# Optimization experiments

Measured on AMD Instinct MI355X. Metric: run time of the kernel, lower is better.

The kernel has to match this reference:

```python
import jax, jax.numpy as jnp
import numpy as np

B, S, D = 4, 2048, 2048
H = 16
HD = D // H  # 128


def setup_inputs() -> dict:
    key = jax.random.key(0)
    ks = jax.random.split(key, 5)
    scale = 1.0 / np.sqrt(D)
    return {
        "x": jax.random.normal(ks[0], (B, S, D), dtype=jnp.float32),
        "wq": jax.random.normal(ks[1], (D, D), dtype=jnp.float32) * scale,
        "wk": jax.random.normal(ks[2], (D, D), dtype=jnp.float32) * scale,
        "wv": jax.random.normal(ks[3], (D, D), dtype=jnp.float32) * scale,
        "wo": jax.random.normal(ks[4], (D, D), dtype=jnp.float32) * scale,
    }


def reference(x, wq, wk, wv, wo):
    # nn.Linear applies x @ W.T
    b, s, d = x.shape
    q = (x @ wq.T).reshape(b, s, H, HD).transpose(0, 2, 1, 3)  # [b,h,s,hd]
    k = (x @ wk.T).reshape(b, s, H, HD).transpose(0, 2, 1, 3)
    v = (x @ wv.T).reshape(b, s, H, HD).transpose(0, 2, 1, 3)
    scores = jnp.einsum('bhqd,bhkd->bhqk', q, k) / np.sqrt(HD)
    causal = jnp.tril(jnp.ones((s, s), dtype=bool))
    scores = jnp.where(causal, scores, -jnp.inf)
    prob = jax.nn.softmax(scores, axis=-1)
    out = jnp.einsum('bhqk,bhkd->bhqd', prob, v)
    out = out.transpose(0, 2, 1, 3).reshape(b, s, d)
    return out @ wo.T
```

## Files before the change

kernel.cpp:

```cpp
#include <hip/hip_runtime.h>


#define B_  4
#define S_  2048
#define D_  2048
#define H_  16
#define HD_ 128

typedef __bf16 bf16x8 __attribute__((ext_vector_type(8)));
typedef float  f32x4  __attribute__((ext_vector_type(4)));

#define OFF_XB  0u
#define OFF_WQ  16777216u
#define OFF_WK  20971520u
#define OFF_WV  25165824u
#define OFF_WO  29360128u
#define OFF_QB  33554432u
#define OFF_KB  50331648u
#define OFF_VT  67108864u
#define OFF_AT  83886080u

#define GLOAD_LDS16(gsrc, ldst)                                                   \
  __builtin_amdgcn_global_load_lds(                                               \
      (const __attribute__((address_space(1))) void*)(gsrc),                      \
      (__attribute__((address_space(3))) void*)(ldst), 16, 0, 0)

#define MFMA16(a, b, cacc) __builtin_amdgcn_mfma_f32_16x16x32_bf16(a, b, cacc, 0, 0, 0)

__device__ __forceinline__ unsigned short f2bfu(float f) {
  unsigned u = __float_as_uint(f);
  return (unsigned short)((u + 0x7fffu + ((u >> 16) & 1u)) >> 16);
}
__device__ __forceinline__ float bfu2f(unsigned short u) {
  return __uint_as_float(((unsigned)u) << 16);
}

__global__ __launch_bounds__(256) void cvt5(const float* __restrict__ x,
                                            const float* __restrict__ wq,
                                            const float* __restrict__ wk,
                                            const float* __restrict__ wv,
                                            const float* __restrict__ wo,
                                            unsigned short* __restrict__ ws) {
  long i = (long)blockIdx.x * 256 + threadIdx.x;
  const float* srcf;
  unsigned short* dst;
  long j;
  if (i < 4194304L)      { srcf = x;  dst = ws + OFF_XB; j = i; }
  else if (i < 5242880L) { srcf = wq; dst = ws + OFF_WQ; j = i - 4194304L; }
  else if (i < 6291456L) { srcf = wk; dst = ws + OFF_WK; j = i - 5242880L; }
  else if (i < 7340032L) { srcf = wv; dst = ws + OFF_WV; j = i - 6291456L; }
  else                   { srcf = wo; dst = ws + OFF_WO; j = i - 7340032L; }
  float4 v = ((const float4*)srcf)[j];
  ushort4 o;
  o.x = f2bfu(v.x); o.y = f2bfu(v.y); o.z = f2bfu(v.z); o.w = f2bfu(v.w);
  ((ushort4*)dst)[j] = o;
}

__device__ __forceinline__ void stage_half(const unsigned short* __restrict__ g,
                                           int Kdim, int rowBase, int k0,
                                           unsigned short* lds, int w, int l) {
#pragma unroll
  for (int rr = 0; rr < 2; rr++) {
    int seg = w + rr * 8;
    int row = seg * 8 + (l >> 3);
    int ccol = ((l & 7) ^ (l >> 3)) * 8;
    GLOAD_LDS16(g + (size_t)(rowBase + row) * Kdim + k0 + ccol, lds + seg * 512);
  }
}

__device__ __forceinline__ bf16x8 lds_frag(const unsigned short* half_, int row,
                                           int s, int g) {
  return *(const bf16x8*)((const char*)half_ + row * 128 +
                          ((s * 64 + g * 16) ^ ((row & 7) << 4)));
}

__device__ __forceinline__ void gemm256(const unsigned short* __restrict__ A,
                                        const unsigned short* __restrict__ Bt,
                                        int rowBase, int colBase, int Kdim,
                                        unsigned short* smem, f32x4 (&acc)[8][4]) {
  const int tid = threadIdx.x, w = tid >> 6, l = tid & 63;
  const int wm = w >> 2, wn = w & 3, c = l & 15, g = l >> 4;
  unsigned short* As = smem;
  unsigned short* Bs = smem + 32768;
  const int NT = Kdim / 64;

#pragma unroll
  for (int i = 0; i < 8; i++)
#pragma unroll
    for (int j = 0; j < 4; j++) acc[i][j] = (f32x4){0.f, 0.f, 0.f, 0.f};

  stage_half(A,  Kdim, rowBase,       0,  As + 0 * 8192, w, l);
  stage_half(Bt, Kdim, colBase,       0,  Bs + 0 * 8192, w, l);
  stage_half(Bt, Kdim, colBase + 128, 0,  Bs + 1 * 8192, w, l);
  stage_half(A,  Kdim, rowBase + 128, 0,  As + 1 * 8192, w, l);
  stage_half(A,  Kdim, rowBase,       64, As + 2 * 8192, w, l);
  stage_half(Bt, Kdim, colBase,       64, Bs + 2 * 8192, w, l);
  stage_half(Bt, Kdim, colBase + 128, 64, Bs + 3 * 8192, w, l);
  asm volatile("s_waitcnt vmcnt(6)" ::: "memory");
  asm volatile("s_barrier" ::: "memory");

  bf16x8 aF[4][2], bF[4][2];

  for (int t = 0; t < NT; ++t) {
    const int par = t & 1;
    const unsigned short* A0h = As + (par * 2 + 0) * 8192;
    const unsigned short* A1h = As + (par * 2 + 1) * 8192;
    const unsigned short* B0h = Bs + (par * 2 + 0) * 8192;
    const unsigned short* B1h = Bs + (par * 2 + 1) * 8192;

#pragma unroll
    for (int m = 0; m < 4; m++) {
      int row = m * 32 + wm * 16 + c;
#pragma unroll
      for (int s = 0; s < 2; s++) aF[m][s] = lds_frag(A0h, row, s, g);
    }
#pragma unroll
    for (int n = 0; n < 2; n++) {
      int row = n * 64 + wn * 16 + c;
#pragma unroll
      for (int s = 0; s < 2; s++) bF[n][s] = lds_frag(B0h, row, s, g);
    }
    if (t + 1 < NT)
      stage_half(A, Kdim, rowBase + 128, (t + 1) * 64,
                 As + (((t + 1) & 1) * 2 + 1) * 8192, w, l);
    asm volatile("s_barrier" ::: "memory");
    __builtin_amdgcn_s_setprio(1);
#pragma unroll
    for (int m = 0; m < 4; m++)
#pragma unroll
      for (int n = 0; n < 2; n++)
#pragma unroll
        for (int s = 0; s < 2; s++) acc[m][n] = MFMA16(aF[m][s], bF[n][s], acc[m][n]);
    __builtin_amdgcn_s_setprio(0);
    asm volatile("s_barrier" ::: "memory");

#pragma unroll
    for (int n = 0; n < 2; n++) {
      int row = n * 64 + wn * 16 + c;
#pragma unroll
      for (int s = 0; s < 2; s++) bF[2 + n][s] = lds_frag(B1h, row, s, g);
    }
    if (t + 2 < NT)
      stage_half(A, Kdim, rowBase, (t + 2) * 64, As + (par * 2 + 0) * 8192, w, l);
    asm volatile("s_barrier" ::: "memory");
    __builtin_amdgcn_s_setprio(1);
#pragma unroll
    for (int m = 0; m < 4; m++)
#pragma unroll
      for (int n = 0; n < 2; n++)
#pragma unroll
        for (int s = 0; s < 2; s++)
          acc[m][2 + n] = MFMA16(aF[m][s], bF[2 + n][s], acc[m][2 + n]);
    __builtin_amdgcn_s_setprio(0);
    asm volatile("s_barrier" ::: "memory");

#pragma unroll
    for (int m = 0; m < 4; m++) {
      int row = m * 32 + wm * 16 + c;
#pragma unroll
      for (int s = 0; s < 2; s++) aF[m][s] = lds_frag(A1h, row, s, g);
    }
    if (t + 2 < NT)
      stage_half(Bt, Kdim, colBase, (t + 2) * 64, Bs + (par * 2 + 0) * 8192, w, l);
    asm volatile("s_barrier" ::: "memory");
    __builtin_amdgcn_s_setprio(1);
#pragma unroll
    for (int m = 0; m < 4; m++)
#pragma unroll
      for (int n = 0; n < 2; n++)
#pragma unroll
        for (int s = 0; s < 2; s++)
          acc[4 + m][2 + n] = MFMA16(aF[m][s], bF[2 + n][s], acc[4 + m][2 + n]);
    __builtin_amdgcn_s_setprio(0);
    asm volatile("s_barrier" ::: "memory");

    if (t + 2 < NT)
      stage_half(Bt, Kdim, colBase + 128, (t + 2) * 64, Bs + (par * 2 + 1) * 8192, w, l);
    asm volatile("s_barrier" ::: "memory");
    __builtin_amdgcn_s_setprio(1);
#pragma unroll
    for (int m = 0; m < 4; m++)
#pragma unroll
      for (int n = 0; n < 2; n++)
#pragma unroll
        for (int s = 0; s < 2; s++)
          acc[4 + m][n] = MFMA16(aF[m][s], bF[n][s], acc[4 + m][n]);
    __builtin_amdgcn_s_setprio(0);
    if (t == NT - 2) asm volatile("s_waitcnt vmcnt(0)" ::: "memory");
    else             asm volatile("s_waitcnt vmcnt(6)" ::: "memory");
    asm volatile("s_barrier" ::: "memory");
  }
}

__global__ __launch_bounds__(512, 2) void qkv_gemm(const unsigned short* __restrict__ xb,
                                                   const unsigned short* __restrict__ wqb,
                                                   const unsigned short* __restrict__ wkb,
                                                   const unsigned short* __restrict__ wvb,
                                                   unsigned short* __restrict__ Qb,
                                                   unsigned short* __restrict__ Kb,
                                                   unsigned short* __restrict__ Vtb) {
  __shared__ __align__(16) unsigned short smem[65536];
  const int tid = threadIdx.x, w = tid >> 6, l = tid & 63;
  const int wm = w >> 2, wn = w & 3, c = l & 15, g = l >> 4;
  const int mat = blockIdx.z;
  const unsigned short* Bt = (mat == 0) ? wqb : (mat == 1) ? wkb : wvb;
  const int rowBase = blockIdx.x * 256, colBase = blockIdx.y * 256;

  f32x4 acc[8][4];
  gemm256(xb, Bt, rowBase, colBase, D_, smem, acc);

  const int b = rowBase / S_;
  const int sBase = rowBase & (S_ - 1);

  if (mat < 2) {
    unsigned short* dstb = (mat == 0 ? Qb : Kb);
    const float scale = (mat == 0) ? 0.08838834764831845f : 1.0f;
#pragma unroll
    for (int mk = 0; mk < 8; mk++)
#pragma unroll
      for (int nk = 0; nk < 4; nk++) {
        int colT = nk * 64 + wn * 16 + c;
        size_t head = (size_t)(b * H_ + blockIdx.y * 2 + (colT >> 7));
        int hd = colT & 127;
        unsigned short* dst = dstb + head * S_ * HD_;
#pragma unroll
        for (int r = 0; r < 4; r++) {
          int s = sBase + mk * 32 + wm * 16 + g * 4 + r;
          dst[(size_t)s * HD_ + hd] = f2bfu(acc[mk][nk][r] * scale);
        }
      }
  } else {
#pragma unroll
    for (int mk = 0; mk < 8; mk++)
#pragma unroll
      for (int nk = 0; nk < 4; nk++) {
        int colT = nk * 64 + wn * 16 + c;
        size_t head = (size_t)(b * H_ + blockIdx.y * 2 + (colT >> 7));
        int hd = colT & 127;
        int s0 = sBase + mk * 32 + wm * 16 + g * 4;
        ushort4 o;
        o.x = f2bfu(acc[mk][nk][0]); o.y = f2bfu(acc[mk][nk][1]);
        o.z = f2bfu(acc[mk][nk][2]); o.w = f2bfu(acc[mk][nk][3]);
        *(ushort4*)&Vtb[(head * HD_ + hd) * S_ + s0] = o;
      }
  }
}

__global__ __launch_bounds__(512, 4) void attn(const unsigned short* __restrict__ Qb,
                                               const unsigned short* __restrict__ Kb,
                                               const unsigned short* __restrict__ Vtb,
                                               unsigned short* __restrict__ atb) {
  const int qt = (S_ / 128 - 1) - blockIdx.x;
  const int bh = blockIdx.y;
  const int tid = threadIdx.x, w = tid >> 6, l = tid & 63;
  const int c = l & 15, g = l >> 4;
  const int q0 = qt * 128;
  const int nkt = 2 * qt + 2;

  __shared__ __align__(16) unsigned short Ks[2][64 * 128];
  __shared__ __align__(16) unsigned short Vs[2][128 * 64];
  __shared__ __align__(16) unsigned short Ps[8][16 * 64];

  const unsigned short* Qh = Qb  + (size_t)bh * S_ * HD_;
  const unsigned short* Kh = Kb  + (size_t)bh * S_ * HD_;
  const unsigned short* Vh = Vtb + (size_t)bh * HD_ * S_;

  bf16x8 qf[4];
  {
    int qrow = q0 + w * 16 + c;
#pragma unroll
    for (int kc = 0; kc < 4; kc++)
      qf[kc] = *(const bf16x8*)&Qh[(size_t)qrow * HD_ + kc * 32 + g * 8];
  }

  f32x4 on[8];
#pragma unroll
  for (int n2 = 0; n2 < 8; n2++) on[n2] = (f32x4){0.f, 0.f, 0.f, 0.f};
  float mrow[4] = {-INFINITY, -INFINITY, -INFINITY, -INFINITY};
  float lrow[4] = {0.f, 0.f, 0.f, 0.f};

  auto STAGE = [&](int buf, int kt) {
    const char* Kt = (const char*)(Kh + (size_t)kt * 64 * HD_);
#pragma unroll
    for (int rr = 0; rr < 2; rr++) {
      int seg = rr * 8 + w;
      {
        int row = seg * 4 + (l >> 4);
        int cbs = ((l & 15) * 16) ^ ((row & 7) << 4);
        GLOAD_LDS16(Kt + row * 256 + cbs, (char*)Ks[buf] + seg * 1024);
      }
      {
        int row = seg * 8 + (l >> 3);
        int cbs = ((l & 7) * 16) ^ ((row & 7) << 4);
        GLOAD_LDS16((const char*)Vh + (size_t)row * (S_ * 2) + kt * 128 + cbs,
                    (char*)Vs[buf] + seg * 1024);
      }
    }
  };

  STAGE(0, 0);
  __syncthreads();

  int cur = 0;
  for (int kt = 0; kt < nkt; ++kt) {
    if (kt + 1 < nkt) STAGE(cur ^ 1, kt + 1);

    if (kt * 64 <= q0 + w * 16 + 15) {
      f32x4 sc[4];
#pragma unroll
      for (int n = 0; n < 4; n++) sc[n] = (f32x4){0.f, 0.f, 0.f, 0.f};
      const char* KsB = (const char*)Ks[cur];
      __builtin_amdgcn_s_setprio(1);
#pragma unroll
      for (int n = 0; n < 4; n++) {
        int row = n * 16 + c;
#pragma unroll
        for (int kc = 0; kc < 4; kc++) {
          bf16x8 kf = *(const bf16x8*)(KsB + row * 256 +
                                       ((kc * 64 + g * 16) ^ ((row & 7) << 4)));
          sc[n] = MFMA16(qf[kc], kf, sc[n]);
        }
      }
      __builtin_amdgcn_s_setprio(0);

      if (kt * 64 + 63 > q0 + w * 16) {
#pragma unroll
        for (int n = 0; n < 4; n++)
#pragma unroll
          for (int r = 0; r < 4; r++) {
            int kk = kt * 64 + n * 16 + c;
            int qg = q0 + w * 16 + g * 4 + r;
            if (kk > qg) sc[n][r] = -INFINITY;
          }
      }

      float mt[4], mn[4], corr[4], rs[4];
#pragma unroll
      for (int r = 0; r < 4; r++) {
        mt[r] = fmaxf(fmaxf(sc[0][r], sc[1][r]), fmaxf(sc[2][r], sc[3][r]));
#pragma unroll
        for (int d = 1; d < 16; d <<= 1) mt[r] = fmaxf(mt[r], __shfl_xor(mt[r], d));
        mn[r]   = fmaxf(mrow[r], mt[r]);
        corr[r] = __expf(mrow[r] - mn[r]);
        mrow[r] = mn[r];
        rs[r]   = 0.f;
      }
#pragma unroll
      for (int n = 0; n < 4; n++)
#pragma unroll
        for (int r = 0; r < 4; r++) {
          float p = __expf(sc[n][r] - mn[r]);
          unsigned short u = f2bfu(p);
          rs[r] += bfu2f(u);
          int prow = g * 4 + r;
          int cbyte = ((n * 16 + c) * 2) ^ ((prow & 7) << 4);
          *(unsigned short*)((char*)Ps[w] + prow * 128 + cbyte) = u;
        }
#pragma unroll
      for (int r = 0; r < 4; r++) {
#pragma unroll
        for (int d = 1; d < 16; d <<= 1) rs[r] += __shfl_xor(rs[r], d);
        lrow[r] = lrow[r] * corr[r] + rs[r];
      }
#pragma unroll
      for (int n2 = 0; n2 < 8; n2++)
#pragma unroll
        for (int r = 0; r < 4; r++) on[n2][r] *= corr[r];

      const char* VsB = (const char*)Vs[cur];
#pragma unroll
      for (int s = 0; s < 2; s++) {
        bf16x8 pa = *(const bf16x8*)((const char*)Ps[w] + c * 128 +
                                     ((s * 64 + g * 16) ^ ((c & 7) << 4)));
        __builtin_amdgcn_s_setprio(1);
#pragma unroll
        for (int n2 = 0; n2 < 8; n2++) {
          int vrow = n2 * 16 + c;
          bf16x8 vb = *(const bf16x8*)(VsB + vrow * 128 +
                                       ((s * 64 + g * 16) ^ ((vrow & 7) << 4)));
          on[n2] = MFMA16(pa, vb, on[n2]);
        }
        __builtin_amdgcn_s_setprio(0);
      }
    }

    __syncthreads();
    cur ^= 1;
  }

  const int b = bh >> 4, h = bh & 15;
  float inv[4];
#pragma unroll
  for (int r = 0; r < 4; r++) inv[r] = 1.f / lrow[r];
#pragma unroll
  for (int n2 = 0; n2 < 8; n2++)
#pragma unroll
    for (int r = 0; r < 4; r++) {
      size_t srow = (size_t)(b * S_ + q0 + w * 16 + g * 4 + r);
      atb[srow * D_ + h * HD_ + n2 * 16 + c] = f2bfu(on[n2][r] * inv[r]);
    }
}

__global__ __launch_bounds__(512, 2) void out_gemm(const unsigned short* __restrict__ atb,
                                                   const unsigned short* __restrict__ wob,
                                                   float* __restrict__ out) {
  __shared__ __align__(16) unsigned short smem[65536];
  const int tid = threadIdx.x, w = tid >> 6, l = tid & 63;
  const int wm = w >> 2, wn = w & 3, c = l & 15, g = l >> 4;
  const int rowBase = blockIdx.x * 256, colBase = blockIdx.y * 256;

  f32x4 acc[8][4];
  gemm256(atb, wob, rowBase, colBase, D_, smem, acc);

#pragma unroll
  for (int mk = 0; mk < 8; mk++)
#pragma unroll
    for (int nk = 0; nk < 4; nk++) {
      int col = colBase + nk * 64 + wn * 16 + c;
#pragma unroll
      for (int r = 0; r < 4; r++) {
        int row = rowBase + mk * 32 + wm * 16 + g * 4 + r;
        out[(size_t)row * D_ + col] = acc[mk][nk][r];
      }
    }
}

extern "C" void kernel_launch(void* const* d_in, const int* in_sizes, int n_in,
                              void* d_out, int out_size, void* d_ws, size_t ws_size,
                              hipStream_t stream) {
  const float* x  = (const float*)d_in[0];
  const float* wq = (const float*)d_in[1];
  const float* wk = (const float*)d_in[2];
  const float* wv = (const float*)d_in[3];
  const float* wo = (const float*)d_in[4];
  unsigned short* ws = (unsigned short*)d_ws;
  float* out = (float*)d_out;

  unsigned short* xb  = ws + OFF_XB;
  unsigned short* wqb = ws + OFF_WQ;
  unsigned short* wkb = ws + OFF_WK;
  unsigned short* wvb = ws + OFF_WV;
  unsigned short* wob = ws + OFF_WO;
  unsigned short* Qb  = ws + OFF_QB;
  unsigned short* Kb  = ws + OFF_KB;
  unsigned short* Vtb = ws + OFF_VT;
  unsigned short* atb = ws + OFF_AT;

  hipLaunchKernelGGL(cvt5, dim3(32768), dim3(256), 0, stream, x, wq, wk, wv, wo, ws);
  hipLaunchKernelGGL(qkv_gemm, dim3(32, 8, 3), dim3(512), 0, stream,
                     xb, wqb, wkb, wvb, Qb, Kb, Vtb);
  hipLaunchKernelGGL(attn, dim3(16, 64), dim3(512), 0, stream, Qb, Kb, Vtb, atb);
  hipLaunchKernelGGL(out_gemm, dim3(32, 8), dim3(512), 0, stream, atb, wob, out);
}
```

Measured before the change: 642.2 us.

## Pair causal query tiles per block, use exp2 softmax with lazy rescaling

Each attention block now handles two query tiles, qt and 15-qt, so every block does about the same amount of causal work, and the grid shrinks from 16x64 to 8x64. The Q projection now folds log2(e) into its scale, so the softmax can use exp2f. The running max and output are rescaled only when some row's new max exceeds the old one by more than 11, which skips most correction multiplies. This trades finer grid parallelism for load balance, and the lazy rescale lets unnormalised values grow by up to 2^11 before correction.

```diff
diff --git a/kernel.cpp b/kernel.cpp
--- a/kernel.cpp
+++ b/kernel.cpp
@@ -214,7 +214,7 @@
 
   if (mat < 2) {
     unsigned short* dstb = (mat == 0 ? Qb : Kb);
-    const float scale = (mat == 0) ? 0.08838834764831845f : 1.0f;
+    const float scale = (mat == 0) ? 0.08838834764831845f * 1.4426950408889634f : 1.0f;
 #pragma unroll
     for (int mk = 0; mk < 8; mk++)
 #pragma unroll
@@ -250,12 +250,9 @@
                                                const unsigned short* __restrict__ Kb,
                                                const unsigned short* __restrict__ Vtb,
                                                unsigned short* __restrict__ atb) {
-  const int qt = (S_ / 128 - 1) - blockIdx.x;
   const int bh = blockIdx.y;
   const int tid = threadIdx.x, w = tid >> 6, l = tid & 63;
   const int c = l & 15, g = l >> 4;
-  const int q0 = qt * 128;
-  const int nkt = 2 * qt + 2;
 
   __shared__ __align__(16) unsigned short Ks[2][64 * 128];
   __shared__ __align__(16) unsigned short Vs[2][128 * 64];
@@ -264,20 +261,6 @@
   const unsigned short* Qh = Qb  + (size_t)bh * S_ * HD_;
   const unsigned short* Kh = Kb  + (size_t)bh * S_ * HD_;
   const unsigned short* Vh = Vtb + (size_t)bh * HD_ * S_;
-
-  bf16x8 qf[4];
-  {
-    int qrow = q0 + w * 16 + c;
-#pragma unroll
-    for (int kc = 0; kc < 4; kc++)
-      qf[kc] = *(const bf16x8*)&Qh[(size_t)qrow * HD_ + kc * 32 + g * 8];
-  }
-
-  f32x4 on[8];
-#pragma unroll
-  for (int n2 = 0; n2 < 8; n2++) on[n2] = (f32x4){0.f, 0.f, 0.f, 0.f};
-  float mrow[4] = {-INFINITY, -INFINITY, -INFINITY, -INFINITY};
-  float lrow[4] = {0.f, 0.f, 0.f, 0.f};
 
   auto STAGE = [&](int buf, int kt) {
     const char* Kt = (const char*)(Kh + (size_t)kt * 64 * HD_);
@@ -298,107 +281,133 @@
     }
   };
 
-  STAGE(0, 0);
-  __syncthreads();
-
-  int cur = 0;
-  for (int kt = 0; kt < nkt; ++kt) {
-    if (kt + 1 < nkt) STAGE(cur ^ 1, kt + 1);
-
-    if (kt * 64 <= q0 + w * 16 + 15) {
-      f32x4 sc[4];
-#pragma unroll
-      for (int n = 0; n < 4; n++) sc[n] = (f32x4){0.f, 0.f, 0.f, 0.f};
-      const char* KsB = (const char*)Ks[cur];
-      __builtin_amdgcn_s_setprio(1);
-#pragma unroll
-      for (int n = 0; n < 4; n++) {
-        int row = n * 16 + c;
-#pragma unroll
-        for (int kc = 0; kc < 4; kc++) {
-          bf16x8 kf = *(const bf16x8*)(KsB + row * 256 +
-                                       ((kc * 64 + g * 16) ^ ((row & 7) << 4)));
-          sc[n] = MFMA16(qf[kc], kf, sc[n]);
-        }
-      }
-      __builtin_amdgcn_s_setprio(0);
-
-      if (kt * 64 + 63 > q0 + w * 16) {
+  for (int half = 0; half < 2; ++half) {
+    const int qt = half ? (int)blockIdx.x : (S_ / 128 - 1) - (int)blockIdx.x;
+    const int q0 = qt * 128;
+    const int nkt = 2 * qt + 2;
+
+    bf16x8 qf[4];
+    {
+      int qrow = q0 + w * 16 + c;
+#pragma unroll
+      for (int kc = 0; kc < 4; kc++)
+        qf[kc] = *(const bf16x8*)&Qh[(size_t)qrow * HD_ + kc * 32 + g * 8];
+    }
+
+    f32x4 on[8];
+#pragma unroll
+    for (int n2 = 0; n2 < 8; n2++) on[n2] = (f32x4){0.f, 0.f, 0.f, 0.f};
+    float mrow[4] = {-INFINITY, -INFINITY, -INFINITY, -INFINITY};
+    float lrow[4] = {0.f, 0.f, 0.f, 0.f};
+
+    STAGE(0, 0);
+    __syncthreads();
+
+    int cur = 0;
+    for (int kt = 0; kt < nkt; ++kt) {
+      if (kt + 1 < nkt) STAGE(cur ^ 1, kt + 1);
+
+      if (kt * 64 <= q0 + w * 16 + 15) {
+        f32x4 sc[4];
+#pragma unroll
+        for (int n = 0; n < 4; n++) sc[n] = (f32x4){0.f, 0.f, 0.f, 0.f};
+        const char* KsB = (const char*)Ks[cur];
+        __builtin_amdgcn_s_setprio(1);
+#pragma unroll
+        for (int n = 0; n < 4; n++) {
+          int row = n * 16 + c;
+#pragma unroll
+          for (int kc = 0; kc < 4; kc++) {
+            bf16x8 kf = *(const bf16x8*)(KsB + row * 256 +
+                                         ((kc * 64 + g * 16) ^ ((row & 7) << 4)));
+            sc[n] = MFMA16(qf[kc], kf, sc[n]);
+          }
+        }
+        __builtin_amdgcn_s_setprio(0);
+
+        if (kt * 64 + 63 > q0 + w * 16) {
+#pragma unroll
+          for (int n = 0; n < 4; n++)
+#pragma unroll
+            for (int r = 0; r < 4; r++) {
+              int kk = kt * 64 + n * 16 + c;
+              int qg = q0 + w * 16 + g * 4 + r;
+              if (kk > qg) sc[n][r] = -INFINITY;
+            }
+        }
+
+        float mt[4];
+#pragma unroll
+        for (int r = 0; r < 4; r++) {
+          mt[r] = fmaxf(fmaxf(sc[0][r], sc[1][r]), fmaxf(sc[2][r], sc[3][r]));
+#pragma unroll
+          for (int d = 1; d < 16; d <<= 1) mt[r] = fmaxf(mt[r], __shfl_xor(mt[r], d));
+        }
+        bool need = (mt[0] > mrow[0] + 11.f) || (mt[1] > mrow[1] + 11.f) ||
+                    (mt[2] > mrow[2] + 11.f) || (mt[3] > mrow[3] + 11.f);
+        if (__any(need)) {
+#pragma unroll
+          for (int r = 0; r < 4; r++) {
+            float mn   = fmaxf(mrow[r], mt[r]);
+            float corr = exp2f(mrow[r] - mn);
+            mrow[r] = mn;
+            lrow[r] *= corr;
+#pragma unroll
+            for (int n2 = 0; n2 < 8; n2++) on[n2][r] *= corr;
+          }
+        }
+        float rs[4] = {0.f, 0.f, 0.f, 0.f};
 #pragma unroll
         for (int n = 0; n < 4; n++)
 #pragma unroll
           for (int r = 0; r < 4; r++) {
-            int kk = kt * 64 + n * 16 + c;
-            int qg = q0 + w * 16 + g * 4 + r;
-            if (kk > qg) sc[n][r] = -INFINITY;
+            float p = exp2f(sc[n][r] - mrow[r]);
+            unsigned short u = f2bfu(p);
+            rs[r] += bfu2f(u);
+            int prow = g * 4 + r;
+            int cbyte = ((n * 16 + c) * 2) ^ ((prow & 7) << 4);
+            *(unsigned short*)((char*)Ps[w] + prow * 128 + cbyte) = u;
           }
-      }
-
-      float mt[4], mn[4], corr[4], rs[4];
+#pragma unroll
+        for (int r = 0; r < 4; r++) {
+#pragma unroll
+          for (int d = 1; d < 16; d <<= 1) rs[r] += __shfl_xor(rs[r], d);
+          lrow[r] += rs[r];
+        }
+
+        const char* VsB = (const char*)Vs[cur];
+#pragma unroll
+        for (int s = 0; s < 2; s++) {
+          bf16x8 pa = *(const bf16x8*)((const char*)Ps[w] + c * 128 +
+                                       ((s * 64 + g * 16) ^ ((c & 7) << 4)));
+          __builtin_amdgcn_s_setprio(1);
+#pragma unroll
+          for (int n2 = 0; n2 < 8; n2++) {
+            int vrow = n2 * 16 + c;
+            bf16x8 vb = *(const bf16x8*)(VsB + vrow * 128 +
+                                         ((s * 64 + g * 16) ^ ((vrow & 7) << 4)));
+            on[n2] = MFMA16(pa, vb, on[n2]);
+          }
+          __builtin_amdgcn_s_setprio(0);
+        }
+      }
+
+      __syncthreads();
+      cur ^= 1;
+    }
+
+    const int b = bh >> 4, h = bh & 15;
+    float inv[4];
+#pragma unroll
+    for (int r = 0; r < 4; r++) inv[r] = 1.f / lrow[r];
+#pragma unroll
+    for (int n2 = 0; n2 < 8; n2++)
 #pragma unroll
       for (int r = 0; r < 4; r++) {
-        mt[r] = fmaxf(fmaxf(sc[0][r], sc[1][r]), fmaxf(sc[2][r], sc[3][r]));
-#pragma unroll
-        for (int d = 1; d < 16; d <<= 1) mt[r] = fmaxf(mt[r], __shfl_xor(mt[r], d));
-        mn[r]   = fmaxf(mrow[r], mt[r]);
-        corr[r] = __expf(mrow[r] - mn[r]);
-        mrow[r] = mn[r];
-        rs[r]   = 0.f;
-      }
-#pragma unroll
-      for (int n = 0; n < 4; n++)
-#pragma unroll
-        for (int r = 0; r < 4; r++) {
-          float p = __expf(sc[n][r] - mn[r]);
-          unsigned short u = f2bfu(p);
-          rs[r] += bfu2f(u);
-          int prow = g * 4 + r;
-          int cbyte = ((n * 16 + c) * 2) ^ ((prow & 7) << 4);
-          *(unsigned short*)((char*)Ps[w] + prow * 128 + cbyte) = u;
-        }
-#pragma unroll
-      for (int r = 0; r < 4; r++) {
-#pragma unroll
-        for (int d = 1; d < 16; d <<= 1) rs[r] += __shfl_xor(rs[r], d);
-        lrow[r] = lrow[r] * corr[r] + rs[r];
-      }
-#pragma unroll
-      for (int n2 = 0; n2 < 8; n2++)
-#pragma unroll
-        for (int r = 0; r < 4; r++) on[n2][r] *= corr[r];
-
-      const char* VsB = (const char*)Vs[cur];
-#pragma unroll
-      for (int s = 0; s < 2; s++) {
-        bf16x8 pa = *(const bf16x8*)((const char*)Ps[w] + c * 128 +
-                                     ((s * 64 + g * 16) ^ ((c & 7) << 4)));
-        __builtin_amdgcn_s_setprio(1);
-#pragma unroll
-        for (int n2 = 0; n2 < 8; n2++) {
-          int vrow = n2 * 16 + c;
-          bf16x8 vb = *(const bf16x8*)(VsB + vrow * 128 +
-                                       ((s * 64 + g * 16) ^ ((vrow & 7) << 4)));
-          on[n2] = MFMA16(pa, vb, on[n2]);
-        }
-        __builtin_amdgcn_s_setprio(0);
-      }
-    }
-
-    __syncthreads();
-    cur ^= 1;
+        size_t srow = (size_t)(b * S_ + q0 + w * 16 + g * 4 + r);
+        atb[srow * D_ + h * HD_ + n2 * 16 + c] = f2bfu(on[n2][r] * inv[r]);
+      }
   }
-
-  const int b = bh >> 4, h = bh & 15;
-  float inv[4];
-#pragma unroll
-  for (int r = 0; r < 4; r++) inv[r] = 1.f / lrow[r];
-#pragma unroll
-  for (int n2 = 0; n2 < 8; n2++)
-#pragma unroll
-    for (int r = 0; r < 4; r++) {
-      size_t srow = (size_t)(b * S_ + q0 + w * 16 + g * 4 + r);
-      atb[srow * D_ + h * HD_ + n2 * 16 + c] = f2bfu(on[n2][r] * inv[r]);
-    }
 }
 
 __global__ __launch_bounds__(512, 2) void out_gemm(const unsigned short* __restrict__ atb,
@@ -449,6 +458,6 @@
   hipLaunchKernelGGL(cvt5, dim3(32768), dim3(256), 0, stream, x, wq, wk, wv, wo, ws);
   hipLaunchKernelGGL(qkv_gemm, dim3(32, 8, 3), dim3(512), 0, stream,
                      xb, wqb, wkb, wvb, Qb, Kb, Vtb);
-  hipLaunchKernelGGL(attn, dim3(16, 64), dim3(512), 0, stream, Qb, Kb, Vtb, atb);
+  hipLaunchKernelGGL(attn, dim3(8, 64), dim3(512), 0, stream, Qb, Kb, Vtb, atb);
   hipLaunchKernelGGL(out_gemm, dim3(32, 8), dim3(512), 0, stream, atb, wob, out);
 }
```

Result: faster. 554.4 us (-13.7%).
